# Optimization experiments

Measured on AMD Instinct MI355X. Metric: run time of the kernel, lower is better.

## Reference

```python
import jax, jax.numpy as jnp
import numpy as np

NX, NY, NZ = 64, 48, 32          # grid_resolution
N = NX * NY * NZ                 # 98304 grid cells
P = 10                           # neighbors_in_radius
D = 3                            # spatial dims
M = 5                            # num_modes (fourier)
BN = 64                          # base_neurons
BN_IN = 8                        # base_neurons_in (output channels)
IN_FEAT = D * (1 + 2 * M)        # 33


def _linear_init(k, fan_in, fan_out):
    s = 1.0 / np.sqrt(fan_in)
    kw, kb = jax.random.split(k)
    W = jax.random.uniform(kw, (fan_in, fan_out), jnp.float32, -s, s)
    b = jax.random.uniform(kb, (fan_out,), jnp.float32, -s, s)
    return W, b


def setup_inputs() -> dict:
    key = jax.random.key(0)
    ks = jax.random.split(key, 6)
    # neighbor point coordinates gathered by ball query: (b, N, P, 3)
    x = jax.random.normal(ks[0], (1, N, P, D), jnp.float32)
    # regular grid coordinates: (b, nx, ny, nz, 3)
    grid = jax.random.normal(ks[1], (1, NX, NY, NZ, D), jnp.float32)
    # fourier frequency buffer: exp(linspace(0, pi, num_modes))
    freqs = jnp.exp(jnp.linspace(0.0, float(np.pi), M)).astype(jnp.float32)
    W1, b1 = _linear_init(ks[2], IN_FEAT, BN)
    W2, b2 = _linear_init(ks[3], BN, BN // 2)
    W3, b3 = _linear_init(ks[4], BN // 2, BN_IN)
    return dict(x=x, grid=grid, freqs=freqs,
                W1=W1, b1=b1, W2=W2, b2=b2, W3=W3, b3=b3)


def _fourier_encode(coords, freqs):
    # coords: (b, N, P, D), freqs: (F,)
    scaled = coords[..., None, :] * freqs[:, None]          # (b, N, P, F, D)
    b, n, p = coords.shape[:3]
    scaled = scaled.reshape(b, n, p, -1)                    # (b, N, P, F*D)
    return jnp.concatenate([jnp.sin(scaled), jnp.cos(scaled)], axis=-1)


def reference(x, grid, freqs, W1, b1, W2, b2, W3, b3):
    gelu = lambda t: jax.nn.gelu(t, approximate=False)  # torch F.gelu default = exact erf
    # Fourier feature encode neighbor coords: (b, N, P, 33)
    facets = jnp.concatenate([x, _fourier_encode(x, freqs)], axis=-1)
    h = gelu(facets @ W1 + b1)                              # (b, N, P, 64)
    h = gelu(h @ W2 + b2)                                   # (b, N, P, 32)
    h = jnp.tanh(h @ W3 + b3)                               # (b, N, P, 8)
    # mask out padded neighbors (zero coords); original uses x-coordinate channel
    mask = (jnp.abs(x[..., 0:1]) > 1e-6).astype(h.dtype)    # (b, N, P, 1)
    out = jnp.sum(h * mask, axis=2)                         # scatter/aggregate -> (b, N, 8)
    out = out.reshape(out.shape[0], NX, NY, NZ, BN_IN)
    return jnp.transpose(out, (0, 4, 1, 2, 3))              # (b, 8, nx, ny, nz)
```

## Files before the change

kernel.cpp:

```cpp
#include <hip/hip_runtime.h>
#include <math.h>

#define NXD 64
#define NYD 48
#define NZD 32
#define NPT (NXD*NYD*NZD)
#define PN  10
#define MF  5
#define H1  64
#define H2  32
#define H3  8

#define PTS_PER_BLOCK 32
#define ROWS_PER_BLOCK (PTS_PER_BLOCK*PN)
#define TILES_PER_WAVE 5

#define A2S 72
#define A3S 40

#define INV2PI 0.15915494309189535f

typedef __attribute__((ext_vector_type(8))) short short8;
typedef __attribute__((ext_vector_type(4))) float f32x4;

static __device__ const unsigned short kSlotTab[32] = {
  2048,    3,   70,  137,  204,  271, 1042, 1109,
  2561, 1176, 1243, 1310,  516,  583,  650,  717,
  2562,  272, 1043, 1110, 1177, 1244, 1311,  517,
    72,  139,  206,  273, 1044, 1111, 1178, 1245 };

__device__ __forceinline__ short f2bf(float f) {
    unsigned u = __float_as_uint(f);
    unsigned r = (u + 0x7fffu + ((u >> 16) & 1u)) >> 16;
    return (short)r;
}

__device__ __forceinline__ unsigned short f2bf_hu(float f) {
    return (unsigned short)((__float_as_uint(f) + 0x8000u) >> 16);
}

__device__ __forceinline__ unsigned pack2_bf16(float lo, float hi) {
    return __builtin_amdgcn_perm(__float_as_uint(hi) + 0x8000u,
                                 __float_as_uint(lo) + 0x8000u, 0x07060302u);
}

__device__ __forceinline__ float gelu_fast(float x) {
    float x2 = x * x;
    float t  = x * (2.3022082f + 0.10294324f * x2);
    float E  = __builtin_amdgcn_exp2f(t);
    return x - x * __builtin_amdgcn_rcpf(E + 1.0f);
}

__device__ __forceinline__ float tanh_fast(float v) {
    float E = __builtin_amdgcn_exp2f(2.8853901f * v);
    return 1.0f - 2.0f * __builtin_amdgcn_rcpf(E + 1.0f);
}

__global__ __launch_bounds__(256) void domino_mfma_kernel(
    const float* __restrict__ x,
    const float* __restrict__ freqs,
    const float* __restrict__ W1,
    const float* __restrict__ b1,
    const float* __restrict__ W2,
    const float* __restrict__ b2,
    const float* __restrict__ W3,
    const float* __restrict__ b3,
    float* __restrict__ out)
{
    __shared__ float obuf[ROWS_PER_BLOCK * 9];
    __shared__ __align__(16) unsigned short a2buf[4][16 * A2S];
    __shared__ __align__(16) unsigned short a3buf[4][16 * A3S];
    __shared__ __align__(16) float mcx[4][16];
    __shared__ __align__(16) float mv32[4][16];

    const int tid  = threadIdx.x;
    const int w    = tid >> 6;
    const int lane = tid & 63;
    const int lr   = lane & 15;
    const int lg   = lane >> 4;

    float fA[8], fB[8], offs[8];
    int   rowidx[8];
    float f4rev;
    {
        float fr[MF];
        #pragma unroll
        for (int m = 0; m < MF; ++m) fr[m] = freqs[m];
        f4rev = fr[4] * INV2PI;
        #pragma unroll
        for (int j = 0; j < 8; ++j) {
            const unsigned e = kSlotTab[lg*8 + j];
            const int row = e & 63, m = (e >> 6) & 7, path = (e >> 9) & 1, ty = (e >> 10) & 3;
            rowidx[j] = row;
            const float fm = fr[m] * INV2PI;
            fA[j]   = (ty != 2 && path == 0) ? fm : 0.0f;
            fB[j]   = (ty != 2 && path == 1) ? fm : 0.0f;
            offs[j] = (ty == 1) ? 0.25f : 0.0f;
        }
    }
    const float rawf = (lg < 3) ? 1.0f : 0.0f;

    short8 B1f[4];
    float  w32[4], bv1[4];
    #pragma unroll
    for (int t1 = 0; t1 < 4; ++t1) {
        #pragma unroll
        for (int j = 0; j < 8; ++j)
            B1f[t1][j] = f2bf(W1[rowidx[j]*H1 + t1*16 + lr]);
        w32[t1] = W1[32*H1 + t1*16 + lr];
        bv1[t1] = b1[t1*16 + lr];
    }
    short8 B2f[2][2];
    float  bv2[2];
    #pragma unroll
    for (int s = 0; s < 2; ++s)
        #pragma unroll
        for (int t2 = 0; t2 < 2; ++t2)
            #pragma unroll
            for (int j = 0; j < 8; ++j)
                B2f[s][t2][j] = f2bf(W2[(s*32 + lg*8 + j)*H2 + t2*16 + lr]);
    #pragma unroll
    for (int t2 = 0; t2 < 2; ++t2) bv2[t2] = b2[t2*16 + lr];

    short8 B3f;
    float  bv3 = (lr < H3) ? b3[lr] : 0.0f;
    #pragma unroll
    for (int j = 0; j < 8; ++j)
        B3f[j] = (lr < H3) ? f2bf(W3[(lg*8 + j)*H3 + lr]) : (short)0;

    const int wrow0 = blockIdx.x * ROWS_PER_BLOCK + w * (TILES_PER_WAVE*16);

    #pragma unroll 1
    for (int t = 0; t < TILES_PER_WAVE; ++t) {
        const int myrow = wrow0 + t*16 + lr;

        const float* xp = x + (size_t)myrow * 3;
        const float cx = xp[0], cy = xp[1], cz = xp[2];

        const float cA = (lg <= 1) ? cx : ((lg == 2) ? cy : cz);
        const float cB = (lg == 0) ? cx : ((lg == 1) ? cy : cz);

        float fv[8];
        #pragma unroll
        for (int j = 0; j < 8; ++j) {
            float rev = cA * fA[j] + (cB * fB[j] + offs[j]);
            fv[j] = __builtin_amdgcn_sinf(__builtin_amdgcn_fractf(rev));
        }
        fv[0] += rawf * (cB - fv[0]);

        if (lg == 0) {
            mcx[w][lr]  = cx;
            mv32[w][lr] = __builtin_amdgcn_sinf(__builtin_amdgcn_fractf(cz * f4rev + 0.25f));
        }

        union { unsigned u[4]; short8 s8; } a1u;
        #pragma unroll
        for (int j = 0; j < 4; ++j) a1u.u[j] = pack2_bf16(fv[2*j], fv[2*j+1]);
        const short8 a1 = a1u.s8;

        f32x4 c1[4];
        #pragma unroll
        for (int t1 = 0; t1 < 4; ++t1) {
            f32x4 ci = {bv1[t1], bv1[t1], bv1[t1], bv1[t1]};
            c1[t1] = __builtin_amdgcn_mfma_f32_16x16x32_bf16(a1, B1f[t1], ci, 0, 0, 0);
        }
        const f32x4 v32r = *(const f32x4*)&mv32[w][lg*4];
        const f32x4 mxr  = *(const f32x4*)&mcx[w][lg*4];
        #pragma unroll
        for (int t1 = 0; t1 < 4; ++t1)
            #pragma unroll
            for (int r = 0; r < 4; ++r)
                c1[t1][r] += v32r[r] * w32[t1];
        #pragma unroll
        for (int t1 = 0; t1 < 4; ++t1)
            #pragma unroll
            for (int r = 0; r < 4; ++r)
                c1[t1][r] = gelu_fast(c1[t1][r]);

        #pragma unroll
        for (int t1 = 0; t1 < 4; ++t1)
            #pragma unroll
            for (int r = 0; r < 4; ++r)
                a2buf[w][(lg*4 + r)*A2S + t1*16 + lr] = f2bf_hu(c1[t1][r]);
        short8 a2f[2];
        #pragma unroll
        for (int s = 0; s < 2; ++s)
            a2f[s] = *(const short8*)&a2buf[w][lr*A2S + s*32 + lg*8];

        f32x4 c2[2];
        #pragma unroll
        for (int t2 = 0; t2 < 2; ++t2) {
            f32x4 ci = {bv2[t2], bv2[t2], bv2[t2], bv2[t2]};
            ci = __builtin_amdgcn_mfma_f32_16x16x32_bf16(a2f[0], B2f[0][t2], ci, 0, 0, 0);
            c2[t2] = __builtin_amdgcn_mfma_f32_16x16x32_bf16(a2f[1], B2f[1][t2], ci, 0, 0, 0);
        }
        #pragma unroll
        for (int t2 = 0; t2 < 2; ++t2)
            #pragma unroll
            for (int r = 0; r < 4; ++r)
                c2[t2][r] = gelu_fast(c2[t2][r]);

        #pragma unroll
        for (int t2 = 0; t2 < 2; ++t2)
            #pragma unroll
            for (int r = 0; r < 4; ++r)
                a3buf[w][(lg*4 + r)*A3S + t2*16 + lr] = f2bf_hu(c2[t2][r]);
        short8 a3f = *(const short8*)&a3buf[w][lr*A3S + lg*8];

        f32x4 c3 = {bv3, bv3, bv3, bv3};
        c3 = __builtin_amdgcn_mfma_f32_16x16x32_bf16(a3f, B3f, c3, 0, 0, 0);

        #pragma unroll
        for (int r = 0; r < 4; ++r) {
            const int brow = w*(TILES_PER_WAVE*16) + t*16 + lg*4 + r;
            const float mk = (fabsf(mxr[r]) > 1e-6f) ? 1.0f : 0.0f;
            if (lr < H3) obuf[brow*9 + lr] = mk * tanh_fast(c3[r]);
        }
    }

    __syncthreads();

    {
        const int p  = tid >> 3;
        const int ch = tid & 7;
        float sum = 0.0f;
        #pragma unroll
        for (int i = 0; i < PN; ++i) sum += obuf[(p*PN + i)*9 + ch];
        const int gp = blockIdx.x * PTS_PER_BLOCK + p;
        out[(size_t)ch * NPT + gp] = sum;
    }
}

extern "C" void kernel_launch(void* const* d_in, const int* in_sizes, int n_in,
                              void* d_out, int out_size, void* d_ws, size_t ws_size,
                              hipStream_t stream) {
    const float* x     = (const float*)d_in[0];
    const float* freqs = (const float*)d_in[2];
    const float* W1    = (const float*)d_in[3];
    const float* b1    = (const float*)d_in[4];
    const float* W2    = (const float*)d_in[5];
    const float* b2    = (const float*)d_in[6];
    const float* W3    = (const float*)d_in[7];
    const float* b3    = (const float*)d_in[8];
    float* out = (float*)d_out;

    const int grid = NPT / PTS_PER_BLOCK;
    domino_mfma_kernel<<<grid, 256, 0, stream>>>(x, freqs, W1, b1, W2, b2, W3, b3, out);
}
```

Baseline: 129.2 us.

## Stage coordinates into LDS via async load, move coefficients to LDS, shrink buffers

Coordinates for each wave are prefetched with a single global_load_lds of 16 bytes per lane into shared memory, replacing the per-tile strided global loads. The per-slot Fourier coefficients move from registers into shared tables, which lowers register pressure. The a3 buffer now reuses a2buf, and the output staging buffer becomes fp16, cutting the LDS footprint, presumably so more blocks fit per CU. The fp16 staging adds rounding error to the summed outputs, and a block-wide sync is added before the main loop.

```diff
diff --git a/kernel.cpp b/kernel.cpp
--- a/kernel.cpp
+++ b/kernel.cpp
@@ -67,11 +67,14 @@
     const float* __restrict__ b3,
     float* __restrict__ out)
 {
-    __shared__ float obuf[ROWS_PER_BLOCK * 9];
     __shared__ __align__(16) unsigned short a2buf[4][16 * A2S];
-    __shared__ __align__(16) unsigned short a3buf[4][16 * A3S];
+    __shared__ __align__(16) float cbuf[976];
+    __shared__ __align__(16) _Float16 obuf[ROWS_PER_BLOCK * 9];
     __shared__ __align__(16) float mcx[4][16];
     __shared__ __align__(16) float mv32[4][16];
+    __shared__ __align__(16) float coefA[2][32];
+    __shared__ __align__(16) float coefB[2][32];
+    __shared__ __align__(16) float coefO[2][32];
 
     const int tid  = threadIdx.x;
     const int w    = tid >> 6;
@@ -79,34 +82,40 @@
     const int lr   = lane & 15;
     const int lg   = lane >> 4;
 
-    float fA[8], fB[8], offs[8];
-    int   rowidx[8];
-    float f4rev;
+    const int wrow0 = blockIdx.x * ROWS_PER_BLOCK + w * (TILES_PER_WAVE*16);
+
+    if (tid < 32) {
+        const unsigned e = kSlotTab[tid];
+        const int m = (e >> 6) & 7, path = (e >> 9) & 1, ty = (e >> 10) & 3;
+        const float fm = freqs[m] * INV2PI;
+        const float fa = (ty != 2 && path == 0) ? fm : 0.0f;
+        const float fb = (ty != 2 && path == 1) ? fm : 0.0f;
+        const float fo = (ty == 1) ? 0.25f : 0.0f;
+        coefA[0][tid] = fa; coefA[1][tid] = fa;
+        coefB[0][tid] = fb; coefB[1][tid] = fb;
+        coefO[0][tid] = fo; coefO[1][tid] = fo;
+    }
+
     {
-        float fr[MF];
-        #pragma unroll
-        for (int m = 0; m < MF; ++m) fr[m] = freqs[m];
-        f4rev = fr[4] * INV2PI;
-        #pragma unroll
-        for (int j = 0; j < 8; ++j) {
-            const unsigned e = kSlotTab[lg*8 + j];
-            const int row = e & 63, m = (e >> 6) & 7, path = (e >> 9) & 1, ty = (e >> 10) & 3;
-            rowidx[j] = row;
-            const float fm = fr[m] * INV2PI;
-            fA[j]   = (ty != 2 && path == 0) ? fm : 0.0f;
-            fB[j]   = (ty != 2 && path == 1) ? fm : 0.0f;
-            offs[j] = (ty == 1) ? 0.25f : 0.0f;
-        }
-    }
-    const float rawf = (lg < 3) ? 1.0f : 0.0f;
+        const int sl = (w == 3 && lane >= 60) ? 59 : lane;
+        const float* gsrc = x + (size_t)wrow0 * 3 + (size_t)sl * 4;
+        __builtin_amdgcn_global_load_lds(
+            (const __attribute__((address_space(1))) void*)gsrc,
+            (__attribute__((address_space(3))) void*)&cbuf[w * 240], 16, 0, 0);
+    }
+
+    const float f4rev = freqs[4] * INV2PI;
+    const float rawf  = (lg < 3) ? 1.0f : 0.0f;
 
     short8 B1f[4];
     float  w32[4], bv1[4];
     #pragma unroll
     for (int t1 = 0; t1 < 4; ++t1) {
         #pragma unroll
-        for (int j = 0; j < 8; ++j)
-            B1f[t1][j] = f2bf(W1[rowidx[j]*H1 + t1*16 + lr]);
+        for (int j = 0; j < 8; ++j) {
+            const int row = kSlotTab[lg*8 + j] & 63;
+            B1f[t1][j] = f2bf(W1[row*H1 + t1*16 + lr]);
+        }
         w32[t1] = W1[32*H1 + t1*16 + lr];
         bv1[t1] = b1[t1*16 + lr];
     }
@@ -128,23 +137,40 @@
     for (int j = 0; j < 8; ++j)
         B3f[j] = (lr < H3) ? f2bf(W3[(lg*8 + j)*H3 + lr]) : (short)0;
 
-    const int wrow0 = blockIdx.x * ROWS_PER_BLOCK + w * (TILES_PER_WAVE*16);
+    __syncthreads();
 
     #pragma unroll 1
     for (int t = 0; t < TILES_PER_WAVE; ++t) {
-        const int myrow = wrow0 + t*16 + lr;
-
-        const float* xp = x + (size_t)myrow * 3;
-        const float cx = xp[0], cy = xp[1], cz = xp[2];
+        const int cfx = w*240 + (t*16 + lr)*3;
+        const float cx = cbuf[cfx + 0];
+        const float cy = cbuf[cfx + 1];
+        const float cz = cbuf[cfx + 2];
 
         const float cA = (lg <= 1) ? cx : ((lg == 2) ? cy : cz);
         const float cB = (lg == 0) ? cx : ((lg == 1) ? cy : cz);
 
+        const int tc = t & 1;
         float fv[8];
-        #pragma unroll
-        for (int j = 0; j < 8; ++j) {
-            float rev = cA * fA[j] + (cB * fB[j] + offs[j]);
-            fv[j] = __builtin_amdgcn_sinf(__builtin_amdgcn_fractf(rev));
+        {
+            const f32x4 fa0 = *(const f32x4*)&coefA[tc][lg*8];
+            const f32x4 fb0 = *(const f32x4*)&coefB[tc][lg*8];
+            const f32x4 fo0 = *(const f32x4*)&coefO[tc][lg*8];
+            #pragma unroll
+            for (int j = 0; j < 4; ++j) {
+                float rev = cA*fa0[j] + (cB*fb0[j] + fo0[j]);
+                fv[j] = __builtin_amdgcn_sinf(__builtin_amdgcn_fractf(rev));
+            }
+        }
+        __builtin_amdgcn_sched_barrier(0);
+        {
+            const f32x4 fa1 = *(const f32x4*)&coefA[tc][lg*8 + 4];
+            const f32x4 fb1 = *(const f32x4*)&coefB[tc][lg*8 + 4];
+            const f32x4 fo1 = *(const f32x4*)&coefO[tc][lg*8 + 4];
+            #pragma unroll
+            for (int j = 0; j < 4; ++j) {
+                float rev = cA*fa1[j] + (cB*fb1[j] + fo1[j]);
+                fv[4+j] = __builtin_amdgcn_sinf(__builtin_amdgcn_fractf(rev));
+            }
         }
         fv[0] += rawf * (cB - fv[0]);
 
@@ -200,12 +226,13 @@
             for (int r = 0; r < 4; ++r)
                 c2[t2][r] = gelu_fast(c2[t2][r]);
 
+        unsigned short* const a3p = &a2buf[w][0];
         #pragma unroll
         for (int t2 = 0; t2 < 2; ++t2)
             #pragma unroll
             for (int r = 0; r < 4; ++r)
-                a3buf[w][(lg*4 + r)*A3S + t2*16 + lr] = f2bf_hu(c2[t2][r]);
-        short8 a3f = *(const short8*)&a3buf[w][lr*A3S + lg*8];
+                a3p[(lg*4 + r)*A3S + t2*16 + lr] = f2bf_hu(c2[t2][r]);
+        short8 a3f = *(const short8*)&a3p[lr*A3S + lg*8];
 
         f32x4 c3 = {bv3, bv3, bv3, bv3};
         c3 = __builtin_amdgcn_mfma_f32_16x16x32_bf16(a3f, B3f, c3, 0, 0, 0);
@@ -214,7 +241,7 @@
         for (int r = 0; r < 4; ++r) {
             const int brow = w*(TILES_PER_WAVE*16) + t*16 + lg*4 + r;
             const float mk = (fabsf(mxr[r]) > 1e-6f) ? 1.0f : 0.0f;
-            if (lr < H3) obuf[brow*9 + lr] = mk * tanh_fast(c3[r]);
+            if (lr < H3) obuf[brow*9 + lr] = (_Float16)(mk * tanh_fast(c3[r]));
         }
     }
 
@@ -225,7 +252,7 @@
         const int ch = tid & 7;
         float sum = 0.0f;
         #pragma unroll
-        for (int i = 0; i < PN; ++i) sum += obuf[(p*PN + i)*9 + ch];
+        for (int i = 0; i < PN; ++i) sum += (float)obuf[(p*PN + i)*9 + ch];
         const int gp = blockIdx.x * PTS_PER_BLOCK + p;
         out[(size_t)ch * NPT + gp] = sum;
     }
```

After: 125.4 us. -2.9%, faster.
